# Optimization experiments

Hardware: AMD Instinct MI355X
Metric: run time of the kernel (lower is better)

The kernel has to match this reference:

```python
import jax, jax.numpy as jnp
import numpy as np
from jax import lax

NUM_HEADS = 8
EPS = 1e-12  # F.normalize default eps


def _l2norm(t):
    # F.normalize(t, dim=-1): t / max(||t||_2, eps)
    n = jnp.sqrt(jnp.sum(t * t, axis=-1, keepdims=True))
    return t / jnp.maximum(n, EPS)


def setup_inputs() -> dict:
    key = jax.random.key(0)
    k1, k2, k3, k4 = jax.random.split(key, 4)
    b, c, h, w = 16, 384, 64, 64
    x = jax.random.normal(k1, (b, c, h, w), dtype=jnp.float32)
    # 1x1 conv weights stored as (out, in); depthwise 3x3 as (3c, 1, 3, 3)
    w_qkv = jax.random.normal(k2, (3 * c, c), dtype=jnp.float32) * (1.0 / np.sqrt(c))
    w_dw = jax.random.normal(k3, (3 * c, 1, 3, 3), dtype=jnp.float32) * (1.0 / 3.0)
    w_proj = jax.random.normal(k4, (c, c), dtype=jnp.float32) * (1.0 / np.sqrt(c))
    temperature = jnp.ones((1, NUM_HEADS, 1, 1), dtype=jnp.float32)
    return {"x": x, "w_qkv": w_qkv, "w_dw": w_dw, "w_proj": w_proj,
            "temperature": temperature}


def reference(x, w_qkv, w_dw, w_proj, temperature):
    b, c, h, w = x.shape
    hw = h * w
    d = c // NUM_HEADS  # per-head channel dim

    # 1x1 pointwise conv: (b,c,h,w) x (3c,c) -> (b,3c,h,w)
    qkv = jnp.einsum('bchw,oc->bohw', x, w_qkv)
    # depthwise 3x3 conv, groups = 3c, padding SAME, no bias
    qkv = lax.conv_general_dilated(
        qkv, w_dw, window_strides=(1, 1), padding='SAME',
        feature_group_count=3 * c,
        dimension_numbers=('NCHW', 'OIHW', 'NCHW'))

    q, k, v = jnp.split(qkv, 3, axis=1)
    q = q.reshape(b, NUM_HEADS, d, hw)
    k = k.reshape(b, NUM_HEADS, d, hw)
    v = v.reshape(b, NUM_HEADS, d, hw)

    q = _l2norm(q)
    k = _l2norm(k)

    # transposed (channel) attention: scores over channel dim, (b,H,d,d)
    scores = jnp.einsum('bhdn,bhen->bhde', q, k) * temperature
    attn = jax.nn.softmax(scores, axis=-1)

    out = jnp.einsum('bhde,bhen->bhdn', attn, v).reshape(b, c, h, w)
    out = jnp.einsum('bchw,oc->bohw', out, w_proj)
    return out
```

## Files before the change

kernel.cpp:

```cpp
#include <hip/hip_runtime.h>
#include <hip/hip_bf16.h>
#include <math.h>

#define B_   16
#define C_   384
#define C3_  1152
#define HW_  4096
#define NH_  8
#define D_   48

typedef _Float16 f16x8 __attribute__((ext_vector_type(8)));
typedef _Float16 f16x4 __attribute__((ext_vector_type(4)));
typedef _Float16 f16x2 __attribute__((ext_vector_type(2)));
typedef float    f32x4 __attribute__((ext_vector_type(4)));

#define ASM_VMCNT(n) asm volatile("s_waitcnt vmcnt(" #n ")" ::: "memory")

__global__ __launch_bounds__(256) void prep_inputs(
    const float* __restrict__ x, _Float16* __restrict__ xt,
    const float* __restrict__ wqkv, const float* __restrict__ wproj,
    _Float16* __restrict__ oq, _Float16* __restrict__ op)
{
    const int t = threadIdx.x;
    if (blockIdx.z == 16) {
        const int nq = C3_ * C_ / 4;
        const int np = C_ * C_ / 4;
        int idx = (blockIdx.y * 64 + blockIdx.x) * 256 + t;
        for (int i = idx; i < nq + np; i += 384 * 256) {
            const float* src; _Float16* dst; int j;
            if (i < nq) { src = wqkv; dst = oq; j = i; }
            else        { src = wproj; dst = op; j = i - nq; }
            float4 v = *(const float4*)&src[(size_t)j * 4];
            f16x4 h = { (_Float16)v.x, (_Float16)v.y, (_Float16)v.z, (_Float16)v.w };
            *(f16x4*)&dst[(size_t)j * 4] = h;
        }
        return;
    }
    const int b  = blockIdx.z;
    const int k0 = blockIdx.y * 64;
    const int n0 = blockIdx.x * 64;
    __shared__ float sm[64][65];
    const float* xb = x + (size_t)b * C_ * HW_;
    _Float16* xtb = xt + (size_t)b * HW_ * C_;
    #pragma unroll
    for (int i = 0; i < 4; ++i) {
        int row = (t >> 4) + i * 16;
        int col = (t & 15) * 4;
        float4 v = *(const float4*)&xb[(size_t)(k0 + row) * HW_ + n0 + col];
        sm[row][col] = v.x; sm[row][col+1] = v.y; sm[row][col+2] = v.z; sm[row][col+3] = v.w;
    }
    __syncthreads();
    #pragma unroll
    for (int i = 0; i < 2; ++i) {
        int nl = (t >> 3) + i * 32;
        int ks = (t & 7) * 8;
        f16x8 h;
        #pragma unroll
        for (int j = 0; j < 8; ++j) h[j] = (_Float16)sm[ks + j][nl];
        *(f16x8*)&xtb[(size_t)(n0 + nl) * C_ + k0 + ks] = h;
    }
}

template<int M, bool F32OUT>
__global__ __launch_bounds__(256, 2) void mfma_gemm(
    const _Float16* __restrict__ Wb,
    const _Float16* __restrict__ XT,
    void* __restrict__ Cv, long long xstride, long long cstride)
{
    constexpr int K = 384;
    constexpr int BK = 32;
    constexpr int NSTEP = K / BK;
    constexpr int MB = M / 128;
    __shared__ _Float16 LDS[36864];
    _Float16* Ash = LDS;
    _Float16* Bsh = LDS + 3 * 128 * BK;

    const int nwg = MB * 16 * B_;
    const int cpx = nwg >> 3;
    const int bid = blockIdx.x;
    const int L   = (bid & 7) * cpx + (bid >> 3);
    const int m0  = (L % MB) * 128;
    const int nb  = L / MB;
    const int n0  = (nb & 15) * 256;
    const int b   = nb >> 4;

    const _Float16* __restrict__ XTb = XT + (size_t)b * xstride;
    const int t = threadIdx.x;
    const int l = t & 63, w = t >> 6;
    const int frow = l & 15, kseg16 = l >> 4;

    auto stage = [&](int d, int kt) {
        const int kk = kt * BK;
        #pragma unroll
        for (int i = 0; i < 2; ++i) {
            const int u = i * 256 + t;
            const int row = u >> 2, slot = u & 3;
            const int scol = slot ^ (row & 3) ^ ((row >> 2) & 1);
            const _Float16* ga = Wb + (size_t)(m0 + row) * K + kk + scol * 8;
            __builtin_amdgcn_global_load_lds(
                (const __attribute__((address_space(1))) void*)ga,
                (__attribute__((address_space(3))) void*)((char*)(Ash + d * 128 * BK) + u * 16),
                16, 0, 0);
        }
        #pragma unroll
        for (int i = 0; i < 4; ++i) {
            const int u = i * 256 + t;
            const int row = u >> 2, slot = u & 3;
            const int scol = slot ^ (row & 3) ^ ((row >> 2) & 1);
            const _Float16* gb = XTb + (size_t)(n0 + row) * K + kk + scol * 8;
            __builtin_amdgcn_global_load_lds(
                (const __attribute__((address_space(1))) void*)gb,
                (__attribute__((address_space(3))) void*)((char*)(Bsh + d * 256 * BK) + u * 16),
                16, 0, 0);
        }
    };

    f32x4 acc[8][4] = {};

    stage(0, 0); stage(1, 1);
    #pragma unroll
    for (int kt = 0; kt < NSTEP; ++kt) {
        const int cur = kt % 3;
        if (kt + 1 < NSTEP) { ASM_VMCNT(6); } else { ASM_VMCNT(0); }
        __builtin_amdgcn_sched_barrier(0);
        __builtin_amdgcn_s_barrier();
        __builtin_amdgcn_sched_barrier(0);
        if (kt + 2 < NSTEP) stage((kt + 2) % 3, kt + 2);

        const _Float16* Abase = &Ash[cur * 128 * BK];
        const _Float16* Bbase = &Bsh[cur * 256 * BK];

        f16x8 bfr[4];
        #pragma unroll
        for (int ni = 0; ni < 4; ++ni) {
            const int rB = w * 64 + ni * 16 + frow;
            const int cs = kseg16 ^ (rB & 3) ^ ((rB >> 2) & 1);
            bfr[ni] = *(const f16x8*)&Bbase[rB * BK + cs * 8];
        }
        f16x8 afb[2];
        {
            const int rA = frow;
            const int cs = kseg16 ^ (rA & 3) ^ ((rA >> 2) & 1);
            afb[0] = *(const f16x8*)&Abase[rA * BK + cs * 8];
        }
        __builtin_amdgcn_sched_group_barrier(0x100, 5, 0);
        __builtin_amdgcn_s_setprio(1);
        #pragma unroll
        for (int mi = 0; mi < 8; ++mi) {
            if (mi + 1 < 8) {
                const int rA = (mi + 1) * 16 + frow;
                const int cs = kseg16 ^ (rA & 3) ^ ((rA >> 2) & 1);
                afb[(mi + 1) & 1] = *(const f16x8*)&Abase[rA * BK + cs * 8];
            }
            #pragma unroll
            for (int ni = 0; ni < 4; ++ni)
                acc[mi][ni] = __builtin_amdgcn_mfma_f32_16x16x32_f16(
                    bfr[ni], afb[mi & 1], acc[mi][ni], 0, 0, 0);
            if (mi + 1 < 8)
                __builtin_amdgcn_sched_group_barrier(0x100, 1, 0);
            __builtin_amdgcn_sched_group_barrier(0x008, 4, 0);
        }
        __builtin_amdgcn_s_setprio(0);
    }

    __syncthreads();
    char* tbase = (char*)LDS + w * 17408;
    if constexpr (!F32OUT) {
        #pragma unroll
        for (int mi = 0; mi < 8; ++mi)
            #pragma unroll
            for (int ni = 0; ni < 4; ++ni) {
                const int row = mi * 16 + (l & 15);
                const int pxl = ni * 16 + (l >> 4) * 4;
                f16x2 lo = { (_Float16)acc[mi][ni][0], (_Float16)acc[mi][ni][1] };
                f16x2 hi = { (_Float16)acc[mi][ni][2], (_Float16)acc[mi][ni][3] };
                *(f16x2*)(tbase + row * 136 + pxl * 2)     = lo;
                *(f16x2*)(tbase + row * 136 + pxl * 2 + 4) = hi;
            }
        asm volatile("s_waitcnt lgkmcnt(0)" ::: "memory");
        __builtin_amdgcn_sched_barrier(0);
        _Float16* Co = (_Float16*)Cv + (size_t)b * cstride;
        #pragma unroll
        for (int j = 0; j < 16; ++j) {
            const int ch = j * 8 + (l >> 3);
            const int px = (l & 7) * 8;
            f16x4 lo = *(const f16x4*)(tbase + ch * 136 + px * 2);
            f16x4 hi = *(const f16x4*)(tbase + ch * 136 + px * 2 + 8);
            f16x8 v;
            #pragma unroll
            for (int q = 0; q < 4; ++q) { v[q] = lo[q]; v[q + 4] = hi[q]; }
            *(f16x8*)&Co[(size_t)(m0 + ch) * HW_ + n0 + w * 64 + px] = v;
        }
    } else {
        float* Co = (float*)Cv + (size_t)b * cstride;
        #pragma unroll
        for (int p = 0; p < 2; ++p) {
            if (p) { asm volatile("s_waitcnt lgkmcnt(0)" ::: "memory");
                     __builtin_amdgcn_sched_barrier(0); }
            #pragma unroll
            for (int mi = 0; mi < 4; ++mi)
                #pragma unroll
                for (int ni = 0; ni < 4; ++ni) {
                    const int row = mi * 16 + (l & 15);
                    const int pxl = ni * 16 + (l >> 4) * 4;
                    float2 lo = make_float2(acc[p * 4 + mi][ni][0], acc[p * 4 + mi][ni][1]);
                    float2 hi = make_float2(acc[p * 4 + mi][ni][2], acc[p * 4 + mi][ni][3]);
                    *(float2*)(tbase + row * 272 + pxl * 4)     = lo;
                    *(float2*)(tbase + row * 272 + pxl * 4 + 8) = hi;
                }
            asm volatile("s_waitcnt lgkmcnt(0)" ::: "memory");
            __builtin_amdgcn_sched_barrier(0);
            #pragma unroll
            for (int j = 0; j < 16; ++j) {
                const int lch = j * 4 + (l >> 4);
                const int ch  = p * 64 + lch;
                const int px  = (l & 15) * 4;
                float2 lo = *(const float2*)(tbase + lch * 272 + px * 4);
                float2 hi = *(const float2*)(tbase + lch * 272 + px * 4 + 8);
                f32x4 v = { lo.x, lo.y, hi.x, hi.y };
                *(f32x4*)&Co[(size_t)(m0 + ch) * HW_ + n0 + w * 64 + px] = v;
            }
        }
    }
}

__global__ __launch_bounds__(256) void dwconv_norm(
    _Float16* __restrict__ buf, const float* __restrict__ wdw,
    float* __restrict__ nqinv, float* __restrict__ nkinv)
{
    const int plane = blockIdx.x;
    const int ch = plane % C3_, b = plane / C3_;
    __shared__ _Float16 smh[64 * 72];
    __shared__ float wsum[4];
    _Float16* g = buf + (size_t)plane * HW_;
    const int t = threadIdx.x;
    #pragma unroll
    for (int i = 0; i < 2; ++i) {
        const int u = i * 256 + t;
        f16x8 v = *(const f16x8*)&g[u * 8];
        *(f16x8*)&smh[(u >> 3) * 72 + (u & 7) * 8] = v;
    }
    float w[9];
    #pragma unroll
    for (int j = 0; j < 9; ++j) w[j] = wdw[ch * 9 + j];
    __syncthreads();
    float ssq = 0.f;
    #pragma unroll
    for (int i = 0; i < 2; ++i) {
        const int u = i * 256 + t;
        const int y = u >> 3, c0 = (u & 7) * 8;
        float r[3][10];
        #pragma unroll
        for (int dy = 0; dy < 3; ++dy) {
            const int yy = y + dy - 1;
            if (yy < 0 || yy > 63) {
                #pragma unroll
                for (int j = 0; j < 10; ++j) r[dy][j] = 0.f;
            } else {
                f16x8 v = *(const f16x8*)&smh[yy * 72 + c0];
                #pragma unroll
                for (int j = 0; j < 8; ++j) r[dy][j + 1] = (float)v[j];
                r[dy][0] = (c0 > 0)  ? (float)smh[yy * 72 + c0 - 1] : 0.f;
                r[dy][9] = (c0 < 56) ? (float)smh[yy * 72 + c0 + 8] : 0.f;
            }
        }
        f16x8 o;
        #pragma unroll
        for (int j = 0; j < 8; ++j) {
            float s = 0.f;
            #pragma unroll
            for (int dy = 0; dy < 3; ++dy)
                #pragma unroll
                for (int dx = 0; dx < 3; ++dx)
                    s = fmaf(w[dy * 3 + dx], r[dy][j + dx], s);
            o[j] = (_Float16)s;
            ssq = fmaf(s, s, ssq);
        }
        *(f16x8*)&g[u * 8] = o;
    }
    if (ch < 2 * C_) {
        #pragma unroll
        for (int m = 1; m < 64; m <<= 1) ssq += __shfl_xor(ssq, m);
        if ((t & 63) == 0) wsum[t >> 6] = ssq;
        __syncthreads();
        if (t == 0) {
            float tot = wsum[0] + wsum[1] + wsum[2] + wsum[3];
            float inv = 1.f / fmaxf(sqrtf(tot), 1e-12f);
            (ch < C_ ? nqinv : nkinv)[b * C_ + (ch % C_)] = inv;
        }
    }
}

__global__ __launch_bounds__(256) void scores_mfma(
    const _Float16* __restrict__ buf, float* __restrict__ sp)
{
    const int bh = blockIdx.x;
    const int ks = blockIdx.y;
    const int b = bh >> 3, h = bh & 7;
    const _Float16* qbase = buf + ((size_t)b * C3_ + (size_t)h * D_) * HW_;
    const _Float16* kbase = qbase + (size_t)C_ * HW_;
    const int t = threadIdx.x, l = t & 63, w = t >> 6;
    const int frow = l & 15, kseg = (l >> 4) * 8;
    const int p0 = ks * 1024 + w * 256;

    f32x4 acc[3][3] = {};
    #pragma unroll 2
    for (int st = 0; st < 8; ++st) {
        const int p = p0 + st * 32 + kseg;
        f16x8 qf[3], kf[3];
        #pragma unroll
        for (int mi = 0; mi < 3; ++mi)
            qf[mi] = *(const f16x8*)&qbase[(size_t)(mi * 16 + frow) * HW_ + p];
        #pragma unroll
        for (int ni = 0; ni < 3; ++ni)
            kf[ni] = *(const f16x8*)&kbase[(size_t)(ni * 16 + frow) * HW_ + p];
        #pragma unroll
        for (int mi = 0; mi < 3; ++mi)
            #pragma unroll
            for (int ni = 0; ni < 3; ++ni)
                acc[mi][ni] = __builtin_amdgcn_mfma_f32_16x16x32_f16(
                    qf[mi], kf[ni], acc[mi][ni], 0, 0, 0);
    }
    __shared__ float red[4][D_ * D_];
    #pragma unroll
    for (int mi = 0; mi < 3; ++mi)
        #pragma unroll
        for (int ni = 0; ni < 3; ++ni)
            #pragma unroll
            for (int r = 0; r < 4; ++r)
                red[w][(mi * 16 + (l >> 4) * 4 + r) * D_ + ni * 16 + (l & 15)] =
                    acc[mi][ni][r];
    __syncthreads();
    float* out = sp + ((size_t)ks * 128 + bh) * (D_ * D_);
    const float* rf = &red[0][0];
    for (int i = t; i < D_ * D_; i += 256)
        out[i] = rf[i] + rf[2304 + i] + rf[4608 + i] + rf[6912 + i];
}

__global__ __launch_bounds__(256) void softmax_k(
    const float* __restrict__ sp, const float* __restrict__ nqinv,
    const float* __restrict__ nkinv, const float* __restrict__ temp,
    float* __restrict__ attn)
{
    const int row = blockIdx.x * 4 + (threadIdx.x >> 6);
    const int bh = row / D_, d = row % D_;
    const int h = bh & 7;
    const int e = threadIdx.x & 63;
    float s = -INFINITY;
    if (e < D_) {
        float raw = 0.f;
        #pragma unroll
        for (int ks = 0; ks < 4; ++ks)
            raw += sp[((size_t)ks * 128 + bh) * (D_ * D_) + d * D_ + e];
        s = raw * nqinv[bh * D_ + d] * nkinv[bh * D_ + e] * temp[h];
    }
    float m = s;
    #pragma unroll
    for (int off = 1; off < 64; off <<= 1) m = fmaxf(m, __shfl_xor(m, off));
    float p = (e < D_) ? expf(s - m) : 0.f;
    float sum = p;
    #pragma unroll
    for (int off = 1; off < 64; off <<= 1) sum += __shfl_xor(sum, off);
    if (e < D_) attn[(size_t)bh * (D_ * D_) + d * D_ + e] = p / sum;
}

__global__ __launch_bounds__(256) void pv_kernel(
    _Float16* __restrict__ buf, const float* __restrict__ attn)
{
    const int b = blockIdx.z, h = blockIdx.y;
    const int p0 = blockIdx.x * 512 + threadIdx.x * 2;
    __shared__ float a4[48][48];
    const float* ab = attn + ((size_t)b * 8 + h) * (D_ * D_);
    for (int i = threadIdx.x; i < D_ * D_; i += 256) ((float*)a4)[i] = ab[i];
    __syncthreads();
    const _Float16* vbase = buf + ((size_t)b * C3_ + 2 * C_ + (size_t)h * D_) * HW_;
    float2 acc[48];
    #pragma unroll
    for (int d = 0; d < 48; ++d) { acc[d].x = 0.f; acc[d].y = 0.f; }
    #pragma unroll 1
    for (int e4 = 0; e4 < 12; ++e4) {
        float2 vv[4];
        #pragma unroll
        for (int j = 0; j < 4; ++j) {
            f16x2 h2 = *(const f16x2*)&vbase[(size_t)(e4 * 4 + j) * HW_ + p0];
            vv[j].x = (float)h2[0]; vv[j].y = (float)h2[1];
        }
        #pragma unroll
        for (int d = 0; d < 48; ++d) {
            float4 a = *(const float4*)&a4[d][e4 * 4];
            acc[d].x = fmaf(a.x, vv[0].x, fmaf(a.y, vv[1].x, fmaf(a.z, vv[2].x, fmaf(a.w, vv[3].x, acc[d].x))));
            acc[d].y = fmaf(a.x, vv[0].y, fmaf(a.y, vv[1].y, fmaf(a.z, vv[2].y, fmaf(a.w, vv[3].y, acc[d].y))));
        }
    }
    _Float16* xt2b = buf + (size_t)b * C3_ * HW_;
    #pragma unroll
    for (int px = 0; px < 2; ++px) {
        f16x8 tmp[6];
        #pragma unroll
        for (int d = 0; d < 48; ++d) tmp[d >> 3][d & 7] = (_Float16)(px ? acc[d].y : acc[d].x);
        f16x8* dst = (f16x8*)&xt2b[(size_t)(p0 + px) * C_ + h * D_];
        #pragma unroll
        for (int j = 0; j < 6; ++j) dst[j] = tmp[j];
    }
}

extern "C" void kernel_launch(void* const* d_in, const int* in_sizes, int n_in,
                              void* d_out, int out_size, void* d_ws, size_t ws_size,
                              hipStream_t stream)
{
    const float* x      = (const float*)d_in[0];
    const float* w_qkv  = (const float*)d_in[1];
    const float* w_dw   = (const float*)d_in[2];
    const float* w_proj = (const float*)d_in[3];
    const float* temp   = (const float*)d_in[4];
    float* out = (float*)d_out;

    _Float16* buf = (_Float16*)d_ws;
    float* nqinv = (float*)(buf + (size_t)B_ * C3_ * HW_);
    float* nkinv = nqinv + 6144;
    float* sp    = nkinv + 6144;
    float* attn  = sp + (size_t)4 * 128 * D_ * D_;
    _Float16* wqkv_h  = (_Float16*)(attn + (size_t)128 * D_ * D_);
    _Float16* wproj_h = wqkv_h + (size_t)C3_ * C_;
    _Float16* xt1     = wproj_h + (size_t)C_ * C_;

    prep_inputs<<<dim3(64, 6, 17), 256, 0, stream>>>(
        x, xt1, w_qkv, w_proj, wqkv_h, wproj_h);

    mfma_gemm<C3_, false><<<dim3(9 * 16 * 16), 256, 0, stream>>>(
        wqkv_h, xt1, buf, (long long)HW_ * C_, (long long)C3_ * HW_);

    dwconv_norm<<<B_ * C3_, 256, 0, stream>>>(buf, w_dw, nqinv, nkinv);

    scores_mfma<<<dim3(128, 4), 256, 0, stream>>>(buf, sp);

    softmax_k<<<1536, 256, 0, stream>>>(sp, nqinv, nkinv, temp, attn);

    pv_kernel<<<dim3(8, 8, 16), 256, 0, stream>>>(buf, attn);

    mfma_gemm<C_, true><<<dim3(3 * 16 * 16), 256, 0, stream>>>(
        wproj_h, buf, out, (long long)C3_ * HW_, (long long)C_ * HW_);
}
```

Before: 264.7 us.

## Shrink GEMM LDS to double buffer and chunk epilogue for three blocks per CU

Replaces the triple-buffered LDS pipeline in the MFMA GEMM with a double buffer. Each next stage is now issued after a barrier at the end of the compute step, so its prefetch no longer overlaps the current step's compute. The epilogue staging is split into smaller chunks so it fits in the reduced LDS. Launch bounds rise to 3 blocks per SM to trade prefetch depth for occupancy. This risks more exposed load latency and extra barriers, and register pressure may cause spills under the tighter bound.

```diff
diff --git a/kernel.cpp b/kernel.cpp
--- a/kernel.cpp
+++ b/kernel.cpp
@@ -62,7 +62,7 @@
 }
 
 template<int M, bool F32OUT>
-__global__ __launch_bounds__(256, 2) void mfma_gemm(
+__global__ __launch_bounds__(256, 3) void mfma_gemm(
     const _Float16* __restrict__ Wb,
     const _Float16* __restrict__ XT,
     void* __restrict__ Cv, long long xstride, long long cstride)
@@ -71,9 +71,9 @@
     constexpr int BK = 32;
     constexpr int NSTEP = K / BK;
     constexpr int MB = M / 128;
-    __shared__ _Float16 LDS[36864];
+    __shared__ _Float16 LDS[24576];
     _Float16* Ash = LDS;
-    _Float16* Bsh = LDS + 3 * 128 * BK;
+    _Float16* Bsh = LDS + 2 * 128 * BK;
 
     const int nwg = MB * 16 * B_;
     const int cpx = nwg >> 3;
@@ -120,12 +120,11 @@
     stage(0, 0); stage(1, 1);
     #pragma unroll
     for (int kt = 0; kt < NSTEP; ++kt) {
-        const int cur = kt % 3;
+        const int cur = kt & 1;
         if (kt + 1 < NSTEP) { ASM_VMCNT(6); } else { ASM_VMCNT(0); }
         __builtin_amdgcn_sched_barrier(0);
         __builtin_amdgcn_s_barrier();
         __builtin_amdgcn_sched_barrier(0);
-        if (kt + 2 < NSTEP) stage((kt + 2) % 3, kt + 2);
 
         const _Float16* Abase = &Ash[cur * 128 * BK];
         const _Float16* Bbase = &Bsh[cur * 256 * BK];
@@ -161,59 +160,71 @@
             __builtin_amdgcn_sched_group_barrier(0x008, 4, 0);
         }
         __builtin_amdgcn_s_setprio(0);
-    }
-
-    __syncthreads();
-    char* tbase = (char*)LDS + w * 17408;
-    if constexpr (!F32OUT) {
-        #pragma unroll
-        for (int mi = 0; mi < 8; ++mi)
-            #pragma unroll
-            for (int ni = 0; ni < 4; ++ni) {
-                const int row = mi * 16 + (l & 15);
-                const int pxl = ni * 16 + (l >> 4) * 4;
-                f16x2 lo = { (_Float16)acc[mi][ni][0], (_Float16)acc[mi][ni][1] };
-                f16x2 hi = { (_Float16)acc[mi][ni][2], (_Float16)acc[mi][ni][3] };
-                *(f16x2*)(tbase + row * 136 + pxl * 2)     = lo;
-                *(f16x2*)(tbase + row * 136 + pxl * 2 + 4) = hi;
-            }
         asm volatile("s_waitcnt lgkmcnt(0)" ::: "memory");
         __builtin_amdgcn_sched_barrier(0);
+        __builtin_amdgcn_s_barrier();
+        if (kt + 2 < NSTEP) stage(cur, kt + 2);
+    }
+
+    __syncthreads();
+    char* tbase = (char*)LDS + w * 8704;
+    if constexpr (!F32OUT) {
         _Float16* Co = (_Float16*)Cv + (size_t)b * cstride;
-        #pragma unroll
-        for (int j = 0; j < 16; ++j) {
-            const int ch = j * 8 + (l >> 3);
-            const int px = (l & 7) * 8;
-            f16x4 lo = *(const f16x4*)(tbase + ch * 136 + px * 2);
-            f16x4 hi = *(const f16x4*)(tbase + ch * 136 + px * 2 + 8);
-            f16x8 v;
-            #pragma unroll
-            for (int q = 0; q < 4; ++q) { v[q] = lo[q]; v[q + 4] = hi[q]; }
-            *(f16x8*)&Co[(size_t)(m0 + ch) * HW_ + n0 + w * 64 + px] = v;
-        }
-    } else {
-        float* Co = (float*)Cv + (size_t)b * cstride;
         #pragma unroll
         for (int p = 0; p < 2; ++p) {
             if (p) { asm volatile("s_waitcnt lgkmcnt(0)" ::: "memory");
                      __builtin_amdgcn_sched_barrier(0); }
             #pragma unroll
-            for (int mi = 0; mi < 4; ++mi)
+            for (int mi2 = 0; mi2 < 4; ++mi2)
                 #pragma unroll
                 for (int ni = 0; ni < 4; ++ni) {
-                    const int row = mi * 16 + (l & 15);
+                    const int mi  = p * 4 + mi2;
+                    const int row = mi2 * 16 + (l & 15);
                     const int pxl = ni * 16 + (l >> 4) * 4;
-                    float2 lo = make_float2(acc[p * 4 + mi][ni][0], acc[p * 4 + mi][ni][1]);
-                    float2 hi = make_float2(acc[p * 4 + mi][ni][2], acc[p * 4 + mi][ni][3]);
+                    f16x2 lo = { (_Float16)acc[mi][ni][0], (_Float16)acc[mi][ni][1] };
+                    f16x2 hi = { (_Float16)acc[mi][ni][2], (_Float16)acc[mi][ni][3] };
+                    *(f16x2*)(tbase + row * 136 + pxl * 2)     = lo;
+                    *(f16x2*)(tbase + row * 136 + pxl * 2 + 4) = hi;
+                }
+            asm volatile("s_waitcnt lgkmcnt(0)" ::: "memory");
+            __builtin_amdgcn_sched_barrier(0);
+            #pragma unroll
+            for (int j = 0; j < 8; ++j) {
+                const int lch = j * 8 + (l >> 3);
+                const int ch  = p * 64 + lch;
+                const int px  = (l & 7) * 8;
+                f16x4 lo = *(const f16x4*)(tbase + lch * 136 + px * 2);
+                f16x4 hi = *(const f16x4*)(tbase + lch * 136 + px * 2 + 8);
+                f16x8 v;
+                #pragma unroll
+                for (int q = 0; q < 4; ++q) { v[q] = lo[q]; v[q + 4] = hi[q]; }
+                *(f16x8*)&Co[(size_t)(m0 + ch) * HW_ + n0 + w * 64 + px] = v;
+            }
+        }
+    } else {
+        float* Co = (float*)Cv + (size_t)b * cstride;
+        #pragma unroll
+        for (int p = 0; p < 4; ++p) {
+            if (p) { asm volatile("s_waitcnt lgkmcnt(0)" ::: "memory");
+                     __builtin_amdgcn_sched_barrier(0); }
+            #pragma unroll
+            for (int mi2 = 0; mi2 < 2; ++mi2)
+                #pragma unroll
+                for (int ni = 0; ni < 4; ++ni) {
+                    const int mi  = p * 2 + mi2;
+                    const int row = mi2 * 16 + (l & 15);
+                    const int pxl = ni * 16 + (l >> 4) * 4;
+                    float2 lo = make_float2(acc[mi][ni][0], acc[mi][ni][1]);
+                    float2 hi = make_float2(acc[mi][ni][2], acc[mi][ni][3]);
                     *(float2*)(tbase + row * 272 + pxl * 4)     = lo;
                     *(float2*)(tbase + row * 272 + pxl * 4 + 8) = hi;
                 }
             asm volatile("s_waitcnt lgkmcnt(0)" ::: "memory");
             __builtin_amdgcn_sched_barrier(0);
             #pragma unroll
-            for (int j = 0; j < 16; ++j) {
+            for (int j = 0; j < 8; ++j) {
                 const int lch = j * 4 + (l >> 4);
-                const int ch  = p * 64 + lch;
+                const int ch  = p * 32 + lch;
                 const int px  = (l & 15) * 4;
                 float2 lo = *(const float2*)(tbase + lch * 272 + px * 4);
                 float2 hi = *(const float2*)(tbase + lch * 272 + px * 4 + 8);
```

Result: slower. 291.6 us (+10.2%).
